# Optimization experiments

Measured on AMD Instinct MI355X. Metric: run time of the kernel, lower is better.

## Reference

```python
import jax, jax.numpy as jnp
import numpy as np

B, E, T = 2, 512, 2048
H = 8
LOCAL_SIZE = 128
NEG_INF = -1e9


def setup_inputs() -> dict:
    key = jax.random.key(0)
    ks = jax.random.split(key, 5)
    return {
        "x": jax.random.normal(ks[0], (B, E, T), dtype=jnp.float32),
        "in_proj_w": jax.random.normal(ks[1], (3 * E, E), dtype=jnp.float32) * (E ** -0.5),
        "in_proj_b": jax.random.normal(ks[2], (3 * E,), dtype=jnp.float32) * 0.02,
        "out_w": jax.random.normal(ks[3], (E, E), dtype=jnp.float32) * (E ** -0.5),
        "out_b": jax.random.normal(ks[4], (E,), dtype=jnp.float32) * 0.02,
    }


def _local_mask(t, local_size, dtype):
    # allowed iff |i - j| <= local_size // 2 (sliding local window)
    i = jnp.arange(t)[:, None]
    j = jnp.arange(t)[None, :]
    allowed = jnp.abs(i - j) <= (local_size // 2)
    return jnp.where(allowed, jnp.zeros((), dtype), jnp.full((), NEG_INF, dtype))


def reference(x, in_proj_w, in_proj_b, out_w, out_b):
    dh = E // H
    scale = 1.0 / jnp.sqrt(jnp.asarray(dh, x.dtype))
    xt = jnp.transpose(x, (0, 2, 1))               # [B, T, E]
    qkv = xt @ in_proj_w.T + in_proj_b             # [B, T, 3E]
    q, k, v = jnp.split(qkv, 3, axis=-1)
    q = q.reshape(B, T, H, dh)
    k = k.reshape(B, T, H, dh)
    v = v.reshape(B, T, H, dh)
    scores = jnp.einsum("bqhd,bkhd->bhqk", q, k) * scale  # [B, H, T, T]
    scores = scores + _local_mask(T, LOCAL_SIZE, scores.dtype)
    attn = jax.nn.softmax(scores, axis=-1)
    ctx = jnp.einsum("bhqk,bkhd->bqhd", attn, v).reshape(B, T, E)
    attn_out = ctx @ out_w.T + out_b               # [B, T, E]
    attn_out = jnp.transpose(attn_out, (0, 2, 1))  # [B, E, T]
    return jax.nn.relu(attn_out * x)
```

## Files before the change

### kernel.cpp

```cpp
#include <hip/hip_runtime.h>
#include <stdint.h>


#define DEVI __device__ __forceinline__

typedef __attribute__((ext_vector_type(8))) short bf16x8;
typedef __attribute__((ext_vector_type(4))) float f32x4;

DEVI unsigned short f2bf(float f) {
  unsigned u = __float_as_uint(f);
  u += 0x7fffu + ((u >> 16) & 1u);
  return (unsigned short)(u >> 16);
}
DEVI float bf2f(unsigned short h) { return __uint_as_float(((unsigned)h) << 16); }

#define GLL16(gp, lp)                                                          \
  __builtin_amdgcn_global_load_lds(                                            \
      (const __attribute__((address_space(1))) void*)(gp),                     \
      (__attribute__((address_space(3))) void*)(lp), 16, 0, 0)

#define MFMA(a, b, c) __builtin_amdgcn_mfma_f32_16x16x32_bf16((a), (b), (c), 0, 0, 0)

__global__ __launch_bounds__(256) void k_transpose_split_x(
    const float* __restrict__ x, unsigned short* __restrict__ xh,
    unsigned short* __restrict__ xl) {
  __shared__ float tile[32][33];
  const int b = blockIdx.z, e0 = blockIdx.y * 32, t0 = blockIdx.x * 32;
  const int j = threadIdx.x & 31, i = threadIdx.x >> 5;
#pragma unroll
  for (int rr = 0; rr < 4; rr++) {
    int e = e0 + i + rr * 8;
    tile[i + rr * 8][j] = x[((size_t)b * 512 + e) * 2048 + t0 + j];
  }
  __syncthreads();
#pragma unroll
  for (int rr = 0; rr < 4; rr++) {
    int t = t0 + i + rr * 8;
    float v = tile[j][i + rr * 8];
    size_t o = ((size_t)b * 2048 + t) * 512 + e0 + j;
    unsigned short hv = f2bf(v);
    xh[o] = hv;
    xl[o] = f2bf(v - bf2f(hv));
  }
}

__global__ __launch_bounds__(256) void k_convert_w(
    const float* __restrict__ w_in, const float* __restrict__ w_out,
    unsigned short* __restrict__ wih, unsigned short* __restrict__ woh) {
  int i = blockIdx.x * 256 + threadIdx.x;
  if (i < 786432) {
    wih[i] = f2bf(w_in[i]);
  } else if (i < 786432 + 262144) {
    int j = i - 786432;
    woh[j] = f2bf(w_out[j]);
  }
}

template <int MT>
__global__ __launch_bounds__(256) void k_gemm_split(
    const unsigned short* __restrict__ Ahg, const unsigned short* __restrict__ Alg,
    const unsigned short* __restrict__ Bhg, const float* __restrict__ bias,
    unsigned short* __restrict__ Qs, unsigned short* __restrict__ Kks,
    unsigned short* __restrict__ Vvs, float* __restrict__ attn_out) {
  const int KD = 512;
  constexpr int AI = MT / 32;
  constexpr int AC = MT / 64;
  __shared__ __align__(16) unsigned short Ah_s[MT * 32];
  __shared__ __align__(16) unsigned short Al_s[MT * 32];
  __shared__ __align__(16) unsigned short Bh_s[128 * 32];
  const int tid = threadIdx.x, lane = tid & 63, w = tid >> 6;
  const int m0 = blockIdx.y * MT, n0 = blockIdx.x * 128;
  const int wm = (w >> 1) * (MT / 2), wn = (w & 1) * 64;

  f32x4 acc[AI][4];
#pragma unroll
  for (int i = 0; i < AI; i++)
#pragma unroll
    for (int j = 0; j < 4; j++) acc[i][j] = (f32x4){0.f, 0.f, 0.f, 0.f};

  const int srw = lane >> 2, sc = (lane & 3) * 8;
  const size_t b0 = (size_t)(n0 + w * 32 + srw) * KD + sc;
  const size_t b1 = b0 + (size_t)16 * KD;
  unsigned short* lB0 = &Bh_s[(w * 32) * 32];
  unsigned short* lB1 = &Bh_s[(w * 32 + 16) * 32];
  size_t aoff[AC];
  unsigned short* lAh[AC];
  unsigned short* lAl[AC];
#pragma unroll
  for (int c = 0; c < AC; c++) {
    int rbase = w * (MT / 4) + c * 16;
    aoff[c] = (size_t)(m0 + rbase + srw) * KD + sc;
    lAh[c] = &Ah_s[rbase * 32];
    lAl[c] = &Al_s[rbase * 32];
  }

  const int fm = lane & 15, fq = (lane >> 4) * 8;

  for (int k0 = 0; k0 < KD; k0 += 32) {
    __syncthreads();
#pragma unroll
    for (int c = 0; c < AC; c++) {
      GLL16(Ahg + aoff[c] + k0, lAh[c]);
      GLL16(Alg + aoff[c] + k0, lAl[c]);
    }
    GLL16(Bhg + b0 + k0, lB0);
    GLL16(Bhg + b1 + k0, lB1);
    __builtin_amdgcn_s_waitcnt(0);
    __syncthreads();

    bf16x8 ah[AI], al[AI], bh[4];
#pragma unroll
    for (int i = 0; i < AI; i++) {
      ah[i] = *(const bf16x8*)&Ah_s[(wm + i * 16 + fm) * 32 + fq];
      al[i] = *(const bf16x8*)&Al_s[(wm + i * 16 + fm) * 32 + fq];
    }
#pragma unroll
    for (int j = 0; j < 4; j++)
      bh[j] = *(const bf16x8*)&Bh_s[(wn + j * 16 + fm) * 32 + fq];
#pragma unroll
    for (int i = 0; i < AI; i++)
#pragma unroll
      for (int j = 0; j < 4; j++) {
        acc[i][j] = MFMA(ah[i], bh[j], acc[i][j]);
        acc[i][j] = MFMA(al[i], bh[j], acc[i][j]);
      }
  }

  const int quad = lane >> 4;
#pragma unroll
  for (int i = 0; i < AI; i++)
#pragma unroll
    for (int j = 0; j < 4; j++) {
      int gn = n0 + wn + j * 16 + fm;
      float bv = bias[gn];
#pragma unroll
      for (int r = 0; r < 4; r++) {
        int gm = m0 + wm + i * 16 + quad * 4 + r;
        float v = acc[i][j][r] + bv;
        if (MT == 128) {
          int bb = gm >> 11, t = gm & 2047;
          int sec = gn >> 9, cc = gn & 511;
          int h = cc >> 6, d = cc & 63;
          if (sec == 0) v *= 0.125f;
          unsigned short* dst = sec == 0 ? Qs : (sec == 1 ? Kks : Vvs);
          dst[(((size_t)(bb * 8 + h)) * 2048 + t) * 64 + d] = f2bf(v);
        } else {
          attn_out[(size_t)gm * 512 + gn] = v;
        }
      }
    }
}

#define KSTR 88
#define VSTR 216
__global__ __launch_bounds__(256) void k_attention(
    const unsigned short* __restrict__ Qs, const unsigned short* __restrict__ Kks,
    const unsigned short* __restrict__ Vvs, unsigned short* __restrict__ ctx_hi,
    unsigned short* __restrict__ ctx_lo) {
  __shared__ __align__(16) unsigned short KP_s[192 * KSTR];
  __shared__ __align__(16) unsigned short Vt_s[64 * VSTR];
  __shared__ float redm[4 * 64];
  __shared__ float reds[4 * 64];

  const int tid = threadIdx.x, lane = tid & 63, w = tid >> 6;
  const int q0 = blockIdx.x * 64;
  const int bh = blockIdx.y;
  const int j0 = q0 - 64;
  const size_t base = (size_t)bh * 2048 * 64;

  for (int idx = tid; idx < 192 * 8; idx += 256) {
    int r = idx >> 3, c = idx & 7;
    int j = j0 + r;
    j = j < 0 ? 0 : (j > 2047 ? 2047 : j);
    uint4 v = *(const uint4*)&Kks[base + (size_t)j * 64 + c * 8];
    *(uint4*)&KP_s[r * KSTR + c * 8] = v;
  }
  for (int idx = tid; idx < 192 * 8; idx += 256) {
    int r = idx >> 3, c8 = (idx & 7) * 8;
    int j = j0 + r;
    uint4 v;
    if (j >= 0 && j < 2048)
      v = *(const uint4*)&Vvs[base + (size_t)j * 64 + c8];
    else
      v = (uint4){0u, 0u, 0u, 0u};
    const unsigned short* e = (const unsigned short*)&v;
#pragma unroll
    for (int u = 0; u < 8; u++) Vt_s[(c8 + u) * VSTR + r] = e[u];
  }

  const int fm = lane & 15, quad = lane >> 4;
  bf16x8 aq[4][2];
#pragma unroll
  for (int mt = 0; mt < 4; mt++)
#pragma unroll
    for (int ks = 0; ks < 2; ks++)
      aq[mt][ks] = *(const bf16x8*)&Qs[base + (size_t)(q0 + mt * 16 + fm) * 64 +
                                       ks * 32 + quad * 8];
  __syncthreads();

  const int n0s = w * 48;
  f32x4 s_acc[4][3];
#pragma unroll
  for (int mt = 0; mt < 4; mt++)
#pragma unroll
    for (int nt = 0; nt < 3; nt++) s_acc[mt][nt] = (f32x4){0.f, 0.f, 0.f, 0.f};
#pragma unroll
  for (int nt = 0; nt < 3; nt++)
#pragma unroll
    for (int ks = 0; ks < 2; ks++) {
      bf16x8 bk =
          *(const bf16x8*)&KP_s[(n0s + nt * 16 + fm) * KSTR + ks * 32 + quad * 8];
#pragma unroll
      for (int mt = 0; mt < 4; mt++) s_acc[mt][nt] = MFMA(aq[mt][ks], bk, s_acc[mt][nt]);
    }

  float rm[4][4];
#pragma unroll
  for (int mt = 0; mt < 4; mt++)
#pragma unroll
    for (int r = 0; r < 4; r++) rm[mt][r] = -1e30f;
#pragma unroll
  for (int mt = 0; mt < 4; mt++)
#pragma unroll
    for (int nt = 0; nt < 3; nt++) {
      int jj = n0s + nt * 16 + fm;
      int jg = j0 + jj;
#pragma unroll
      for (int r = 0; r < 4; r++) {
        int ii = mt * 16 + quad * 4 + r;
        bool ok = (jj >= ii) && (jj <= ii + 128) && (jg >= 0) && (jg < 2048);
        float sv = ok ? s_acc[mt][nt][r] : -1e30f;
        s_acc[mt][nt][r] = sv;
        rm[mt][r] = fmaxf(rm[mt][r], sv);
      }
    }
#pragma unroll
  for (int off = 1; off < 16; off <<= 1)
#pragma unroll
    for (int mt = 0; mt < 4; mt++)
#pragma unroll
      for (int r = 0; r < 4; r++)
        rm[mt][r] = fmaxf(rm[mt][r], __shfl_xor(rm[mt][r], off));
  if (fm == 0)
#pragma unroll
    for (int mt = 0; mt < 4; mt++)
#pragma unroll
      for (int r = 0; r < 4; r++)
        redm[w * 64 + mt * 16 + quad * 4 + r] = rm[mt][r];
  __syncthreads();
  float fmx[4][4];
#pragma unroll
  for (int mt = 0; mt < 4; mt++)
#pragma unroll
    for (int r = 0; r < 4; r++) {
      int row = mt * 16 + quad * 4 + r;
      fmx[mt][r] = fmaxf(fmaxf(redm[row], redm[64 + row]),
                         fmaxf(redm[128 + row], redm[192 + row]));
    }
  float rs[4][4];
#pragma unroll
  for (int mt = 0; mt < 4; mt++)
#pragma unroll
    for (int r = 0; r < 4; r++) rs[mt][r] = 0.f;
#pragma unroll
  for (int mt = 0; mt < 4; mt++)
#pragma unroll
    for (int nt = 0; nt < 3; nt++)
#pragma unroll
      for (int r = 0; r < 4; r++) {
        float e = __expf(s_acc[mt][nt][r] - fmx[mt][r]);
        s_acc[mt][nt][r] = e;
        rs[mt][r] += e;
      }
#pragma unroll
  for (int off = 1; off < 16; off <<= 1)
#pragma unroll
    for (int mt = 0; mt < 4; mt++)
#pragma unroll
      for (int r = 0; r < 4; r++) rs[mt][r] += __shfl_xor(rs[mt][r], off);
  if (fm == 0)
#pragma unroll
    for (int mt = 0; mt < 4; mt++)
#pragma unroll
      for (int r = 0; r < 4; r++)
        reds[w * 64 + mt * 16 + quad * 4 + r] = rs[mt][r];
  __syncthreads();
  float inv[4][4];
#pragma unroll
  for (int mt = 0; mt < 4; mt++)
#pragma unroll
    for (int r = 0; r < 4; r++) {
      int row = mt * 16 + quad * 4 + r;
      inv[mt][r] =
          1.0f / (reds[row] + reds[64 + row] + reds[128 + row] + reds[192 + row]);
    }
#pragma unroll
  for (int mt = 0; mt < 4; mt++)
#pragma unroll
    for (int nt = 0; nt < 3; nt++) {
      int col = n0s + nt * 16 + fm;
#pragma unroll
      for (int r = 0; r < 4; r++) {
        int row = mt * 16 + quad * 4 + r;
        KP_s[row * VSTR + col] = f2bf(s_acc[mt][nt][r] * inv[mt][r]);
      }
    }
  __syncthreads();

  const int n0v = w * 16;
  f32x4 o_acc[4];
#pragma unroll
  for (int mt = 0; mt < 4; mt++) o_acc[mt] = (f32x4){0.f, 0.f, 0.f, 0.f};
#pragma unroll
  for (int ks = 0; ks < 6; ks++) {
    bf16x8 bv = *(const bf16x8*)&Vt_s[(n0v + fm) * VSTR + ks * 32 + quad * 8];
#pragma unroll
    for (int mt = 0; mt < 4; mt++) {
      bf16x8 ap = *(const bf16x8*)&KP_s[(mt * 16 + fm) * VSTR + ks * 32 + quad * 8];
      o_acc[mt] = MFMA(ap, bv, o_acc[mt]);
    }
  }
  const int bb = bh >> 3, h = bh & 7;
#pragma unroll
  for (int mt = 0; mt < 4; mt++)
#pragma unroll
    for (int r = 0; r < 4; r++) {
      int t = q0 + mt * 16 + quad * 4 + r;
      int c = h * 64 + n0v + fm;
      float v = o_acc[mt][r];
      unsigned short hv = f2bf(v);
      size_t o = ((size_t)(bb * 2048 + t)) * 512 + c;
      ctx_hi[o] = hv;
      ctx_lo[o] = f2bf(v - bf2f(hv));
    }
}

__global__ __launch_bounds__(256) void k_final(const float* __restrict__ attn,
                                               const float* __restrict__ x,
                                               float* __restrict__ out) {
  __shared__ float tile[32][33];
  const int b = blockIdx.z, e0 = blockIdx.y * 32, t0 = blockIdx.x * 32;
  const int j = threadIdx.x & 31, i = threadIdx.x >> 5;
#pragma unroll
  for (int rr = 0; rr < 4; rr++) {
    int t = t0 + i + rr * 8;
    tile[i + rr * 8][j] = attn[((size_t)b * 2048 + t) * 512 + e0 + j];
  }
  __syncthreads();
#pragma unroll
  for (int rr = 0; rr < 4; rr++) {
    int e = e0 + i + rr * 8;
    size_t o = ((size_t)b * 512 + e) * 2048 + t0 + j;
    float v = tile[j][i + rr * 8] * x[o];
    out[o] = fmaxf(v, 0.f);
  }
}

extern "C" void kernel_launch(void* const* d_in, const int* in_sizes, int n_in,
                              void* d_out, int out_size, void* d_ws, size_t ws_size,
                              hipStream_t stream) {
  const float* x = (const float*)d_in[0];
  const float* w_in = (const float*)d_in[1];
  const float* b_in = (const float*)d_in[2];
  const float* w_out = (const float*)d_in[3];
  const float* b_out = (const float*)d_in[4];
  float* out = (float*)d_out;

  uint8_t* ws = (uint8_t*)d_ws;
  unsigned short* xT_hi = (unsigned short*)(ws + 0);
  unsigned short* xT_lo = (unsigned short*)(ws + 4194304);
  unsigned short* wih   = (unsigned short*)(ws + 8388608);
  unsigned short* woh   = (unsigned short*)(ws + 9961472);
  unsigned short* Qs    = (unsigned short*)(ws + 12582912);
  unsigned short* Kk    = (unsigned short*)(ws + 16777216);
  unsigned short* Vv    = (unsigned short*)(ws + 20971520);
  unsigned short* ctxh  = (unsigned short*)(ws + 25165824);
  unsigned short* ctxl  = (unsigned short*)(ws + 29360128);
  float* attnf          = (float*)(ws + 33554432);

  k_transpose_split_x<<<dim3(64, 16, 2), 256, 0, stream>>>(x, xT_hi, xT_lo);
  k_convert_w<<<4096, 256, 0, stream>>>(w_in, w_out, wih, woh);
  k_gemm_split<128><<<dim3(12, 32), 256, 0, stream>>>(xT_hi, xT_lo, wih, b_in,
                                                      Qs, Kk, Vv, nullptr);
  k_attention<<<dim3(32, 16), 256, 0, stream>>>(Qs, Kk, Vv, ctxh, ctxl);
  k_gemm_split<64><<<dim3(4, 64), 256, 0, stream>>>(ctxh, ctxl, woh, b_out,
                                                    nullptr, nullptr, nullptr,
                                                    attnf);
  k_final<<<dim3(64, 16, 2), 256, 0, stream>>>(attnf, x, out);
}
```

Baseline: 131.6 us.

## Fuse weight conversion into prep kernel and epilogue into output GEMM

Merges the weight-to-bf16 conversion into the x transpose/split kernel as extra grid rows, using float4 vectorized loads. Fuses the final transpose, multiply by x and ReLU into the output-projection GEMM epilogue through a shared-memory tile that aliases the staging buffers. This removes two kernel launches and the fp32 round trip of the intermediate attention output through global memory. In exchange the output GEMM uses more LDS for the 64x129 float tile, which may lower occupancy.

New measurement: 126.1 us. 1.04x faster.

```diff
diff --git a/kernel.cpp b/kernel.cpp
--- a/kernel.cpp
+++ b/kernel.cpp
@@ -21,12 +21,35 @@
 
 #define MFMA(a, b, c) __builtin_amdgcn_mfma_f32_16x16x32_bf16((a), (b), (c), 0, 0, 0)
 
-__global__ __launch_bounds__(256) void k_transpose_split_x(
-    const float* __restrict__ x, unsigned short* __restrict__ xh,
-    unsigned short* __restrict__ xl) {
+__global__ __launch_bounds__(256) void k_prep(
+    const float* __restrict__ x, const float* __restrict__ w_in,
+    const float* __restrict__ w_out, unsigned short* __restrict__ xh,
+    unsigned short* __restrict__ xl, unsigned short* __restrict__ wih,
+    unsigned short* __restrict__ woh) {
+  const int tid = threadIdx.x;
+  if (blockIdx.y == 16) {
+    int cb = (blockIdx.z << 6) | blockIdx.x;
+    const float* src;
+    unsigned short* dst;
+    int base;
+    if (cb < 96) {
+      src = w_in; dst = wih; base = cb * 8192;
+    } else {
+      src = w_out; dst = woh; base = (cb - 96) * 8192;
+    }
+#pragma unroll
+    for (int k = 0; k < 8; k++) {
+      int idx = base + (k * 256 + tid) * 4;
+      float4 v = *(const float4*)&src[idx];
+      ushort4 o;
+      o.x = f2bf(v.x); o.y = f2bf(v.y); o.z = f2bf(v.z); o.w = f2bf(v.w);
+      *(ushort4*)&dst[idx] = o;
+    }
+    return;
+  }
   __shared__ float tile[32][33];
   const int b = blockIdx.z, e0 = blockIdx.y * 32, t0 = blockIdx.x * 32;
-  const int j = threadIdx.x & 31, i = threadIdx.x >> 5;
+  const int j = tid & 31, i = tid >> 5;
 #pragma unroll
   for (int rr = 0; rr < 4; rr++) {
     int e = e0 + i + rr * 8;
@@ -44,37 +67,22 @@
   }
 }
 
-__global__ __launch_bounds__(256) void k_convert_w(
-    const float* __restrict__ w_in, const float* __restrict__ w_out,
-    unsigned short* __restrict__ wih, unsigned short* __restrict__ woh) {
-  int i = blockIdx.x * 256 + threadIdx.x;
-  if (i < 786432) {
-    wih[i] = f2bf(w_in[i]);
-  } else if (i < 786432 + 262144) {
-    int j = i - 786432;
-    woh[j] = f2bf(w_out[j]);
-  }
-}
-
-template <int MT>
-__global__ __launch_bounds__(256) void k_gemm_split(
+__global__ __launch_bounds__(256) void k_gemm_qkv(
     const unsigned short* __restrict__ Ahg, const unsigned short* __restrict__ Alg,
     const unsigned short* __restrict__ Bhg, const float* __restrict__ bias,
     unsigned short* __restrict__ Qs, unsigned short* __restrict__ Kks,
-    unsigned short* __restrict__ Vvs, float* __restrict__ attn_out) {
+    unsigned short* __restrict__ Vvs) {
   const int KD = 512;
-  constexpr int AI = MT / 32;
-  constexpr int AC = MT / 64;
-  __shared__ __align__(16) unsigned short Ah_s[MT * 32];
-  __shared__ __align__(16) unsigned short Al_s[MT * 32];
+  __shared__ __align__(16) unsigned short Ah_s[128 * 32];
+  __shared__ __align__(16) unsigned short Al_s[128 * 32];
   __shared__ __align__(16) unsigned short Bh_s[128 * 32];
   const int tid = threadIdx.x, lane = tid & 63, w = tid >> 6;
-  const int m0 = blockIdx.y * MT, n0 = blockIdx.x * 128;
-  const int wm = (w >> 1) * (MT / 2), wn = (w & 1) * 64;
-
-  f32x4 acc[AI][4];
-#pragma unroll
-  for (int i = 0; i < AI; i++)
+  const int m0 = blockIdx.y * 128, n0 = blockIdx.x * 128;
+  const int wm = (w >> 1) * 64, wn = (w & 1) * 64;
+
+  f32x4 acc[4][4];
+#pragma unroll
+  for (int i = 0; i < 4; i++)
 #pragma unroll
     for (int j = 0; j < 4; j++) acc[i][j] = (f32x4){0.f, 0.f, 0.f, 0.f};
 
@@ -83,42 +91,35 @@
   const size_t b1 = b0 + (size_t)16 * KD;
   unsigned short* lB0 = &Bh_s[(w * 32) * 32];
   unsigned short* lB1 = &Bh_s[(w * 32 + 16) * 32];
-  size_t aoff[AC];
-  unsigned short* lAh[AC];
-  unsigned short* lAl[AC];
-#pragma unroll
-  for (int c = 0; c < AC; c++) {
-    int rbase = w * (MT / 4) + c * 16;
-    aoff[c] = (size_t)(m0 + rbase + srw) * KD + sc;
-    lAh[c] = &Ah_s[rbase * 32];
-    lAl[c] = &Al_s[rbase * 32];
-  }
+  const size_t a0 = (size_t)(m0 + w * 32 + srw) * KD + sc;
+  const size_t a1 = a0 + (size_t)16 * KD;
+  unsigned short* lAh0 = &Ah_s[(w * 32) * 32];
+  unsigned short* lAh1 = &Ah_s[(w * 32 + 16) * 32];
+  unsigned short* lAl0 = &Al_s[(w * 32) * 32];
+  unsigned short* lAl1 = &Al_s[(w * 32 + 16) * 32];
 
   const int fm = lane & 15, fq = (lane >> 4) * 8;
 
   for (int k0 = 0; k0 < KD; k0 += 32) {
     __syncthreads();
-#pragma unroll
-    for (int c = 0; c < AC; c++) {
-      GLL16(Ahg + aoff[c] + k0, lAh[c]);
-      GLL16(Alg + aoff[c] + k0, lAl[c]);
-    }
+    GLL16(Ahg + a0 + k0, lAh0);
+    GLL16(Ahg + a1 + k0, lAh1);
+    GLL16(Alg + a0 + k0, lAl0);
+    GLL16(Alg + a1 + k0, lAl1);
     GLL16(Bhg + b0 + k0, lB0);
     GLL16(Bhg + b1 + k0, lB1);
     __builtin_amdgcn_s_waitcnt(0);
     __syncthreads();
 
-    bf16x8 ah[AI], al[AI], bh[4];
-#pragma unroll
-    for (int i = 0; i < AI; i++) {
+    bf16x8 ah[4], al[4], bh[4];
+#pragma unroll
+    for (int i = 0; i < 4; i++) {
       ah[i] = *(const bf16x8*)&Ah_s[(wm + i * 16 + fm) * 32 + fq];
       al[i] = *(const bf16x8*)&Al_s[(wm + i * 16 + fm) * 32 + fq];
-    }
-#pragma unroll
-    for (int j = 0; j < 4; j++)
-      bh[j] = *(const bf16x8*)&Bh_s[(wn + j * 16 + fm) * 32 + fq];
-#pragma unroll
-    for (int i = 0; i < AI; i++)
+      bh[i] = *(const bf16x8*)&Bh_s[(wn + i * 16 + fm) * 32 + fq];
+    }
+#pragma unroll
+    for (int i = 0; i < 4; i++)
 #pragma unroll
       for (int j = 0; j < 4; j++) {
         acc[i][j] = MFMA(ah[i], bh[j], acc[i][j]);
@@ -128,27 +129,111 @@
 
   const int quad = lane >> 4;
 #pragma unroll
-  for (int i = 0; i < AI; i++)
+  for (int i = 0; i < 4; i++)
 #pragma unroll
     for (int j = 0; j < 4; j++) {
       int gn = n0 + wn + j * 16 + fm;
       float bv = bias[gn];
+      int sec = gn >> 9, cc = gn & 511;
+      int h = cc >> 6, d = cc & 63;
+      unsigned short* dst = sec == 0 ? Qs : (sec == 1 ? Kks : Vvs);
+      float mul = sec == 0 ? 0.125f : 1.0f;
 #pragma unroll
       for (int r = 0; r < 4; r++) {
         int gm = m0 + wm + i * 16 + quad * 4 + r;
-        float v = acc[i][j][r] + bv;
-        if (MT == 128) {
-          int bb = gm >> 11, t = gm & 2047;
-          int sec = gn >> 9, cc = gn & 511;
-          int h = cc >> 6, d = cc & 63;
-          if (sec == 0) v *= 0.125f;
-          unsigned short* dst = sec == 0 ? Qs : (sec == 1 ? Kks : Vvs);
-          dst[(((size_t)(bb * 8 + h)) * 2048 + t) * 64 + d] = f2bf(v);
-        } else {
-          attn_out[(size_t)gm * 512 + gn] = v;
-        }
-      }
-    }
+        int bb = gm >> 11, t = gm & 2047;
+        float v = (acc[i][j][r] + bv) * mul;
+        dst[(((size_t)(bb * 8 + h)) * 2048 + t) * 64 + d] = f2bf(v);
+      }
+    }
+}
+
+__global__ __launch_bounds__(256) void k_gemm_out(
+    const unsigned short* __restrict__ Ahg, const unsigned short* __restrict__ Alg,
+    const unsigned short* __restrict__ Bhg, const float* __restrict__ bias,
+    const float* __restrict__ x, float* __restrict__ out) {
+  const int KD = 512;
+  __shared__ __align__(16) union {
+    struct {
+      unsigned short Ah[64 * 32];
+      unsigned short Al[64 * 32];
+      unsigned short Bh[128 * 32];
+    } st;
+    float tile[64][129];
+  } u;
+  const int tid = threadIdx.x, lane = tid & 63, w = tid >> 6;
+  const int m0 = blockIdx.y * 64, n0 = blockIdx.x * 128;
+  const int wm = (w >> 1) * 32, wn = (w & 1) * 64;
+
+  f32x4 acc[2][4];
+#pragma unroll
+  for (int i = 0; i < 2; i++)
+#pragma unroll
+    for (int j = 0; j < 4; j++) acc[i][j] = (f32x4){0.f, 0.f, 0.f, 0.f};
+
+  const int srw = lane >> 2, sc = (lane & 3) * 8;
+  const size_t b0 = (size_t)(n0 + w * 32 + srw) * KD + sc;
+  const size_t b1 = b0 + (size_t)16 * KD;
+  const size_t a0 = (size_t)(m0 + w * 16 + srw) * KD + sc;
+  unsigned short* lB0 = &u.st.Bh[(w * 32) * 32];
+  unsigned short* lB1 = &u.st.Bh[(w * 32 + 16) * 32];
+  unsigned short* lAh0 = &u.st.Ah[(w * 16) * 32];
+  unsigned short* lAl0 = &u.st.Al[(w * 16) * 32];
+
+  const int fm = lane & 15, fq = (lane >> 4) * 8;
+
+  for (int k0 = 0; k0 < KD; k0 += 32) {
+    __syncthreads();
+    GLL16(Ahg + a0 + k0, lAh0);
+    GLL16(Alg + a0 + k0, lAl0);
+    GLL16(Bhg + b0 + k0, lB0);
+    GLL16(Bhg + b1 + k0, lB1);
+    __builtin_amdgcn_s_waitcnt(0);
+    __syncthreads();
+
+    bf16x8 ah[2], al[2], bh[4];
+#pragma unroll
+    for (int i = 0; i < 2; i++) {
+      ah[i] = *(const bf16x8*)&u.st.Ah[(wm + i * 16 + fm) * 32 + fq];
+      al[i] = *(const bf16x8*)&u.st.Al[(wm + i * 16 + fm) * 32 + fq];
+    }
+#pragma unroll
+    for (int j = 0; j < 4; j++)
+      bh[j] = *(const bf16x8*)&u.st.Bh[(wn + j * 16 + fm) * 32 + fq];
+#pragma unroll
+    for (int i = 0; i < 2; i++)
+#pragma unroll
+      for (int j = 0; j < 4; j++) {
+        acc[i][j] = MFMA(ah[i], bh[j], acc[i][j]);
+        acc[i][j] = MFMA(al[i], bh[j], acc[i][j]);
+      }
+  }
+
+  __syncthreads();
+  const int quad = lane >> 4;
+#pragma unroll
+  for (int i = 0; i < 2; i++)
+#pragma unroll
+    for (int j = 0; j < 4; j++) {
+      int ln = wn + j * 16 + fm;
+      float bv = bias[n0 + ln];
+#pragma unroll
+      for (int r = 0; r < 4; r++) {
+        int lm = wm + i * 16 + quad * 4 + r;
+        u.tile[lm][ln] = acc[i][j][r] + bv;
+      }
+    }
+  __syncthreads();
+
+  const int bb = m0 >> 11, t0 = m0 & 2047;
+  const int tt = tid & 63, e0w = tid >> 6;
+#pragma unroll
+  for (int k = 0; k < 32; k++) {
+    int ee = e0w + k * 4;
+    size_t o = ((size_t)bb * 512 + n0 + ee) * 2048 + t0 + tt;
+    float v = u.tile[tt][ee] * x[o];
+    out[o] = fmaxf(v, 0.f);
+  }
 }
 
 #define KSTR 88
@@ -185,7 +270,7 @@
       v = (uint4){0u, 0u, 0u, 0u};
     const unsigned short* e = (const unsigned short*)&v;
 #pragma unroll
-    for (int u = 0; u < 8; u++) Vt_s[(c8 + u) * VSTR + r] = e[u];
+    for (int uu = 0; uu < 8; uu++) Vt_s[(c8 + uu) * VSTR + r] = e[uu];
   }
 
   const int fm = lane & 15, quad = lane >> 4;
@@ -333,27 +418,6 @@
       ctx_hi[o] = hv;
       ctx_lo[o] = f2bf(v - bf2f(hv));
     }
-}
-
-__global__ __launch_bounds__(256) void k_final(const float* __restrict__ attn,
-                                               const float* __restrict__ x,
-                                               float* __restrict__ out) {
-  __shared__ float tile[32][33];
-  const int b = blockIdx.z, e0 = blockIdx.y * 32, t0 = blockIdx.x * 32;
-  const int j = threadIdx.x & 31, i = threadIdx.x >> 5;
-#pragma unroll
-  for (int rr = 0; rr < 4; rr++) {
-    int t = t0 + i + rr * 8;
-    tile[i + rr * 8][j] = attn[((size_t)b * 2048 + t) * 512 + e0 + j];
-  }
-  __syncthreads();
-#pragma unroll
-  for (int rr = 0; rr < 4; rr++) {
-    int e = e0 + i + rr * 8;
-    size_t o = ((size_t)b * 512 + e) * 2048 + t0 + j;
-    float v = tile[j][i + rr * 8] * x[o];
-    out[o] = fmaxf(v, 0.f);
-  }
 }
 
 extern "C" void kernel_launch(void* const* d_in, const int* in_sizes, int n_in,
@@ -376,15 +440,11 @@
   unsigned short* Vv    = (unsigned short*)(ws + 20971520);
   unsigned short* ctxh  = (unsigned short*)(ws + 25165824);
   unsigned short* ctxl  = (unsigned short*)(ws + 29360128);
-  float* attnf          = (float*)(ws + 33554432);
-
-  k_transpose_split_x<<<dim3(64, 16, 2), 256, 0, stream>>>(x, xT_hi, xT_lo);
-  k_convert_w<<<4096, 256, 0, stream>>>(w_in, w_out, wih, woh);
-  k_gemm_split<128><<<dim3(12, 32), 256, 0, stream>>>(xT_hi, xT_lo, wih, b_in,
-                                                      Qs, Kk, Vv, nullptr);
+
+  k_prep<<<dim3(64, 17, 2), 256, 0, stream>>>(x, w_in, w_out, xT_hi, xT_lo,
+                                              wih, woh);
+  k_gemm_qkv<<<dim3(12, 32), 256, 0, stream>>>(xT_hi, xT_lo, wih, b_in,
+                                               Qs, Kk, Vv);
   k_attention<<<dim3(32, 16), 256, 0, stream>>>(Qs, Kk, Vv, ctxh, ctxl);
-  k_gemm_split<64><<<dim3(4, 64), 256, 0, stream>>>(ctxh, ctxl, woh, b_out,
-                                                    nullptr, nullptr, nullptr,
-                                                    attnf);
-  k_final<<<dim3(64, 16, 2), 256, 0, stream>>>(attnf, x, out);
-}
+  k_gemm_out<<<dim3(4, 64), 256, 0, stream>>>(ctxh, ctxl, woh, b_out, x, out);
+}
```
